# Performance work log

Hardware: AMD Instinct MI355X
Metric: run time of the kernel (lower is better)

Reference implementation:

```python
import jax, jax.numpy as jnp
import numpy as np

B, S, E, H = 64, 512, 768, 256


def setup_inputs() -> dict:
    key = jax.random.key(0)
    ks = jax.random.split(key, 9)
    sc = 0.02  # small init so relu-activated LSTM stays numerically sane
    x = jax.random.normal(ks[0], (B, S, E), dtype=jnp.float32)
    kernel_f = jax.random.normal(ks[1], (E, 4 * H), dtype=jnp.float32) * sc
    rec_f = jax.random.normal(ks[2], (H, 4 * H), dtype=jnp.float32) * sc
    bias_f = jnp.zeros((4 * H,), dtype=jnp.float32)
    kernel_b = jax.random.normal(ks[3], (E, 4 * H), dtype=jnp.float32) * sc
    rec_b = jax.random.normal(ks[4], (H, 4 * H), dtype=jnp.float32) * sc
    bias_b = jnp.zeros((4 * H,), dtype=jnp.float32)
    Wd = jax.random.normal(ks[5], (S * H, 2), dtype=jnp.float32) * sc
    bd = jnp.zeros((2,), dtype=jnp.float32)
    return {"x": x, "kernel_f": kernel_f, "rec_f": rec_f, "bias_f": bias_f,
            "kernel_b": kernel_b, "rec_b": rec_b, "bias_b": bias_b,
            "Wd": Wd, "bd": bd}


def _lstm_relu(x, kernel, rec, bias):
    # Keras LSTM with activation='relu', recurrent_activation='sigmoid'.
    # Gate order in keras kernel: [i, f, c, o].
    b, h = x.shape[0], rec.shape[0]
    xz = jnp.einsum('bse,eg->bsg', x, kernel) + bias  # [B,S,4H] precomputed input part

    def step(carry, zt):
        hp, cp = carry
        z = zt + hp @ rec  # [B,4H]
        zi, zf, zc, zo = jnp.split(z, 4, axis=-1)
        i = jax.nn.sigmoid(zi)
        f = jax.nn.sigmoid(zf)
        o = jax.nn.sigmoid(zo)
        c = f * cp + i * jax.nn.relu(zc)
        hn = o * jax.nn.relu(c)
        return (hn, c), hn

    init = (jnp.zeros((b, h), x.dtype), jnp.zeros((b, h), x.dtype))
    _, hs = jax.lax.scan(step, init, jnp.swapaxes(xz, 0, 1))  # [S,B,H]
    return jnp.swapaxes(hs, 0, 1)  # [B,S,H]


def reference(x, kernel_f, rec_f, bias_f, kernel_b, rec_b, bias_b, Wd, bd):
    h_fwd = _lstm_relu(x, kernel_f, rec_f, bias_f)
    # backward direction: process reversed sequence, reverse output back, then merge_mode='sum'
    h_bwd = _lstm_relu(x[:, ::-1], kernel_b, rec_b, bias_b)[:, ::-1]
    h = h_fwd + h_bwd  # [B,S,H]
    # dropout is identity at inference (training=None)
    flat = h.reshape(h.shape[0], -1)  # [B, S*H]
    logits = flat @ Wd + bd  # [B,2]
    return logits
```

## Files before the change

### kernel.cpp

```cpp
#include <hip/hip_runtime.h>
#include <hip/hip_bf16.h>
#include <hip/hip_fp16.h>

#define B_ 64
#define S_ 512
#define E_ 768
#define H_ 256
#define G_ 1024
#define MROWS 32768

typedef float f32x4 __attribute__((ext_vector_type(4)));
typedef float f32x16 __attribute__((ext_vector_type(16)));
typedef short short8 __attribute__((ext_vector_type(8)));
typedef _Float16 v2h __attribute__((ext_vector_type(2)));
typedef unsigned int u32x4 __attribute__((ext_vector_type(4)));


__global__ void cast_x_kernel(const float* __restrict__ x, __hip_bfloat16* __restrict__ xbf, int n) {
    int i = (blockIdx.x * 256 + threadIdx.x) * 4;
    if (i >= n) return;
    float4 v = *(const float4*)(x + i);
    xbf[i + 0] = __float2bfloat16(v.x);
    xbf[i + 1] = __float2bfloat16(v.y);
    xbf[i + 2] = __float2bfloat16(v.z);
    xbf[i + 3] = __float2bfloat16(v.w);
}

__global__ void prep_kT_kernel(const float* __restrict__ kf, const float* __restrict__ kb,
                               __hip_bfloat16* __restrict__ kT) {
    int idx = blockIdx.x * 256 + threadIdx.x;
    int dir = blockIdx.y;
    const float* src = dir ? kb : kf;
    int k = idx >> 10;
    int n = idx & 1023;
    float v = src[idx];
    kT[(size_t)dir * G_ * E_ + (size_t)n * E_ + k] = __float2bfloat16(v);
}

__global__ void prep_recQ_kernel(const float* __restrict__ rf, const float* __restrict__ rb,
                                 unsigned int* __restrict__ recQ) {
    int idx = blockIdx.x * 256 + threadIdx.x;
    int dir = blockIdx.y;
    const float* src = dir ? rb : rf;
    int g  = idx & 1023;
    int u  = (idx >> 10) & 3;
    int kk = idx >> 12;
    int k0 = 8 * kk + 2 * u;
    float a = src[(size_t)k0 * G_ + g];
    float b = src[(size_t)(k0 + 1) * G_ + g];
    v2h p;
    p[0] = (_Float16)a;
    p[1] = (_Float16)b;
    recQ[(size_t)dir * 131072 + (size_t)kk * 4096 + g * 4 + u] = __builtin_bit_cast(unsigned int, p);
}

#define TM 128
#define TN 128
#define BK 32
#define LDA 40

__global__ __launch_bounds__(256) void gemm_xz_kernel(
        const __hip_bfloat16* __restrict__ xbf,
        const __hip_bfloat16* __restrict__ kT,
        const float* __restrict__ bias_f, const float* __restrict__ bias_b,
        __hip_bfloat16* __restrict__ xz) {
    int dir  = blockIdx.z;
    int nblk = blockIdx.x;
    int mblk = blockIdx.y;
    int tid  = threadIdx.x;
    int wave = tid >> 6, lane = tid & 63;

    __shared__ __hip_bfloat16 shA[TM * LDA];
    __shared__ __hip_bfloat16 shB[TN * LDA];

    int m0 = mblk * TM;
    int n0 = nblk * TN;

    int rowl0 = tid >> 2;
    int rowl1 = rowl0 + 64;
    int k8    = (tid & 3) * 8;
    int ar0 = m0 + rowl0, ar1 = m0 + rowl1;
    int sa0 = (ar0 & ~511) | (dir ? (511 - (ar0 & 511)) : (ar0 & 511));
    int sa1 = (ar1 & ~511) | (dir ? (511 - (ar1 & 511)) : (ar1 & 511));
    const __hip_bfloat16* kbase = kT + (size_t)dir * G_ * E_;

    f32x16 acc[4] = {};

    int lm = lane & 31;
    int kq = (lane >> 5) * 8;

    for (int k0 = 0; k0 < E_; k0 += BK) {
        __syncthreads();
        *(short8*)&shA[rowl0 * LDA + k8] = *(const short8*)(xbf + (size_t)sa0 * E_ + k0 + k8);
        *(short8*)&shA[rowl1 * LDA + k8] = *(const short8*)(xbf + (size_t)sa1 * E_ + k0 + k8);
        *(short8*)&shB[rowl0 * LDA + k8] = *(const short8*)(kbase + (size_t)(n0 + rowl0) * E_ + k0 + k8);
        *(short8*)&shB[rowl1 * LDA + k8] = *(const short8*)(kbase + (size_t)(n0 + rowl1) * E_ + k0 + k8);
        __syncthreads();

#pragma unroll
        for (int kk = 0; kk < BK; kk += 16) {
            short8 afrag = *(const short8*)&shA[(wave * 32 + lm) * LDA + kk + kq];
#pragma unroll
            for (int j = 0; j < 4; ++j) {
                short8 bfrag = *(const short8*)&shB[(j * 32 + lm) * LDA + kk + kq];
                acc[j] = __builtin_amdgcn_mfma_f32_32x32x16_bf16(afrag, bfrag, acc[j], 0, 0, 0);
            }
        }
    }

    const float* bias = dir ? bias_b : bias_f;
#pragma unroll
    for (int j = 0; j < 4; ++j) {
        int col = n0 + j * 32 + lm;
        float bv = bias[col];
#pragma unroll
        for (int reg = 0; reg < 16; ++reg) {
            int row = m0 + wave * 32 + (reg & 3) + 8 * (reg >> 2) + 4 * (lane >> 5);
            xz[((size_t)dir * MROWS + row) * G_ + col] = __float2bfloat16(acc[j][reg] + bv);
        }
    }
}

__device__ inline float dot2f16(unsigned int rbits, unsigned int hbits, float acc) {
#if __has_builtin(__builtin_amdgcn_fdot2)
    return __builtin_amdgcn_fdot2(__builtin_bit_cast(v2h, rbits),
                                  __builtin_bit_cast(v2h, hbits), acc, false);
#else
    v2h r = __builtin_bit_cast(v2h, rbits);
    v2h h = __builtin_bit_cast(v2h, hbits);
    return acc + (float)r[0] * (float)h[0] + (float)r[1] * (float)h[1];
#endif
}

__device__ inline float sigmoidf(float x) { return 1.f / (1.f + __expf(-x)); }

#define KKREG 24
#define KKLDS 8
__global__ __launch_bounds__(512) void scan_kernel(
        const __hip_bfloat16* __restrict__ xz,
        const uint4* __restrict__ recQ,
        const float* __restrict__ Wd,
        const float* __restrict__ bd,
        float* __restrict__ out) {
    int b = blockIdx.x, dir = blockIdx.y, tid = threadIdx.x;
    __shared__ __align__(16) uint4 sh_rec[KKLDS * G_];
    __shared__ __align__(16) _Float16 sh_h[2][H_];
    __shared__ float sh_z[G_];
    __shared__ float rbuf[8];

    const uint4* rqbase = recQ + (size_t)dir * 32768;

    u32x4 rr0[KKREG], rr1[KKREG];
    {
        unsigned long long a0 = (unsigned long long)(const void*)(rqbase + tid);
        unsigned long long a1 = (unsigned long long)(const void*)(rqbase + tid + 512);
#pragma unroll
        for (int kk = 0; kk < KKREG; ++kk) {
            unsigned long long ka0 = a0 + (unsigned long long)kk * 16384ull;
            unsigned long long ka1 = a1 + (unsigned long long)kk * 16384ull;
            asm volatile("global_load_dwordx4 %0, %1, off" : "=v"(rr0[kk]) : "v"(ka0));
            asm volatile("global_load_dwordx4 %0, %1, off" : "=v"(rr1[kk]) : "v"(ka1));
        }
        asm volatile("s_waitcnt vmcnt(0)" ::: "memory");
    }

#pragma unroll
    for (int j = 0; j < KKLDS * 2; ++j)
        sh_rec[j * 512 + tid] = rqbase[KKREG * 1024 + j * 512 + tid];

    if (tid < H_) { sh_h[0][tid] = (_Float16)0.f; }
    float c = 0.f, pl0 = 0.f, pl1 = 0.f;
    const __hip_bfloat16* xzb = xz + ((size_t)dir * MROWS + (size_t)b * S_) * G_ + tid;
    __syncthreads();

    int p = 0;
    for (int s = 0; s < S_; ++s) {
        float xz0 = __bfloat162float(xzb[(size_t)s * G_]);
        float xz1 = __bfloat162float(xzb[(size_t)s * G_ + 512]);
        float2 wv = {0.f, 0.f};
        int t = dir ? (S_ - 1 - s) : s;
        if (tid < H_) wv = ((const float2*)Wd)[t * H_ + tid];

        const uint4* hp = (const uint4*)&sh_h[p][0];
        float z0a = 0.f, z0b = 0.f, z1a = 0.f, z1b = 0.f;

#pragma unroll
        for (int kk = 0; kk < KKREG; ++kk) {
            uint4 hv = hp[kk];
            u32x4 r0 = rr0[kk];
            u32x4 r1 = rr1[kk];
            z0a = dot2f16(r0.x, hv.x, z0a); z0b = dot2f16(r0.y, hv.y, z0b);
            z0a = dot2f16(r0.z, hv.z, z0a); z0b = dot2f16(r0.w, hv.w, z0b);
            z1a = dot2f16(r1.x, hv.x, z1a); z1b = dot2f16(r1.y, hv.y, z1b);
            z1a = dot2f16(r1.z, hv.z, z1a); z1b = dot2f16(r1.w, hv.w, z1b);
        }
#pragma unroll
        for (int j = 0; j < KKLDS; ++j) {
            uint4 hv = hp[KKREG + j];
            uint4 r0 = sh_rec[j * 1024 + tid];
            uint4 r1 = sh_rec[j * 1024 + tid + 512];
            z0a = dot2f16(r0.x, hv.x, z0a); z0b = dot2f16(r0.y, hv.y, z0b);
            z0a = dot2f16(r0.z, hv.z, z0a); z0b = dot2f16(r0.w, hv.w, z0b);
            z1a = dot2f16(r1.x, hv.x, z1a); z1b = dot2f16(r1.y, hv.y, z1b);
            z1a = dot2f16(r1.z, hv.z, z1a); z1b = dot2f16(r1.w, hv.w, z1b);
        }
        sh_z[tid]       = z0a + z0b + xz0;
        sh_z[tid + 512] = z1a + z1b + xz1;
        __syncthreads();

        if (tid < H_) {
            float zi = sh_z[tid];
            float zf = sh_z[H_ + tid];
            float zc = sh_z[2 * H_ + tid];
            float zo = sh_z[3 * H_ + tid];
            float ig = sigmoidf(zi);
            float fg = sigmoidf(zf);
            float og = sigmoidf(zo);
            float cc = fmaxf(zc, 0.f);
            c = fg * c + ig * cc;
            float h = og * fmaxf(c, 0.f);
            sh_h[p ^ 1][tid] = (_Float16)h;

            pl0 = fmaf(h, wv.x, pl0);
            pl1 = fmaf(h, wv.y, pl1);
        }
        __syncthreads();
        p ^= 1;
    }

    if (tid < H_) {
#pragma unroll
        for (int off = 32; off > 0; off >>= 1) {
            pl0 += __shfl_down(pl0, off);
            pl1 += __shfl_down(pl1, off);
        }
    }
    if (tid < H_ && (tid & 63) == 0) {
        int w = tid >> 6;
        rbuf[w] = pl0; rbuf[4 + w] = pl1;
    }
    __syncthreads();
    if (tid == 0) {
        float t0 = rbuf[0] + rbuf[1] + rbuf[2] + rbuf[3];
        float t1 = rbuf[4] + rbuf[5] + rbuf[6] + rbuf[7];
        atomicAdd(&out[b * 2 + 0], t0);
        atomicAdd(&out[b * 2 + 1], t1);
    }
    if (dir == 0 && tid < 2) atomicAdd(&out[b * 2 + tid], bd[tid]);
}

extern "C" void kernel_launch(void* const* d_in, const int* in_sizes, int n_in,
                              void* d_out, int out_size, void* d_ws, size_t ws_size,
                              hipStream_t stream) {
    const float* x        = (const float*)d_in[0];
    const float* kernel_f = (const float*)d_in[1];
    const float* rec_f    = (const float*)d_in[2];
    const float* bias_f   = (const float*)d_in[3];
    const float* kernel_b = (const float*)d_in[4];
    const float* rec_b    = (const float*)d_in[5];
    const float* bias_b   = (const float*)d_in[6];
    const float* Wd       = (const float*)d_in[7];
    const float* bd       = (const float*)d_in[8];
    float* out = (float*)d_out;

    char* w = (char*)d_ws;
    __hip_bfloat16* xz  = (__hip_bfloat16*)w;
    __hip_bfloat16* xbf = (__hip_bfloat16*)(w + 134217728);
    __hip_bfloat16* kT  = (__hip_bfloat16*)(w + 184549376);
    unsigned int*  recQ = (unsigned int*) (w + 187695104);

    int nx = B_ * S_ * E_;
    cast_x_kernel<<<nx / (256 * 4), 256, 0, stream>>>(x, xbf, nx);
    prep_kT_kernel<<<dim3((E_ * G_) / 256, 2), 256, 0, stream>>>(kernel_f, kernel_b, kT);
    prep_recQ_kernel<<<dim3(131072 / 256, 2), 256, 0, stream>>>(rec_f, rec_b, recQ);

    gemm_xz_kernel<<<dim3(G_ / TN, MROWS / TM, 2), 256, 0, stream>>>(xbf, kT, bias_f, bias_b, xz);

    hipMemsetAsync(d_out, 0, (size_t)out_size * sizeof(float), stream);
    scan_kernel<<<dim3(B_, 2), 512, 0, stream>>>(xz, (const uint4*)recQ, Wd, bd, out);
}
```

Measured before the change: 1.191 ms.

## Compute all four gates per thread in scan, pinning weights in AGPRs

The recurrent scan block shrinks from 512 to 256 threads, and each thread now computes all four gate pre-activations for one hidden unit. This removes the sh_z shared-memory exchange and one of the two barriers per timestep. To hold the larger per-thread weight slice, it is split across VGPRs (11 k-chunks), AGPRs accessed through inline accvgpr write/read (14 chunks), and LDS (7 chunks), which cuts LDS reads of weights. The cost is twice as many dot products per thread on half the threads, plus an extra accvgpr read before each AGPR-held weight is used.

```diff
diff --git a/kernel.cpp b/kernel.cpp
--- a/kernel.cpp
+++ b/kernel.cpp
@@ -134,108 +134,145 @@
 
 __device__ inline float sigmoidf(float x) { return 1.f / (1.f + __expf(-x)); }
 
-#define KKREG 24
-#define KKLDS 8
-__global__ __launch_bounds__(512) void scan_kernel(
+__device__ inline unsigned apin(unsigned v) {
+    unsigned a;
+    asm volatile("v_accvgpr_write_b32 %0, %1" : "=a"(a) : "v"(v));
+    return a;
+}
+__device__ inline unsigned aread(unsigned a) {
+    unsigned v;
+    asm volatile("v_accvgpr_read_b32 %0, %1" : "=v"(v) : "a"(a));
+    return v;
+}
+
+#define KKV 11
+#define KKA 14
+#define KKL 7
+__global__ __launch_bounds__(256) __attribute__((amdgpu_waves_per_eu(1)))
+void scan_kernel(
         const __hip_bfloat16* __restrict__ xz,
         const uint4* __restrict__ recQ,
         const float* __restrict__ Wd,
         const float* __restrict__ bd,
         float* __restrict__ out) {
     int b = blockIdx.x, dir = blockIdx.y, tid = threadIdx.x;
-    __shared__ __align__(16) uint4 sh_rec[KKLDS * G_];
+    __shared__ __align__(16) uint4 sh_rec[KKL * G_];
     __shared__ __align__(16) _Float16 sh_h[2][H_];
-    __shared__ float sh_z[G_];
     __shared__ float rbuf[8];
 
     const uint4* rqbase = recQ + (size_t)dir * 32768;
 
-    u32x4 rr0[KKREG], rr1[KKREG];
+    u32x4 vi[KKV], vf[KKV], vc[KKV], vo[KKV];
     {
-        unsigned long long a0 = (unsigned long long)(const void*)(rqbase + tid);
-        unsigned long long a1 = (unsigned long long)(const void*)(rqbase + tid + 512);
-#pragma unroll
-        for (int kk = 0; kk < KKREG; ++kk) {
-            unsigned long long ka0 = a0 + (unsigned long long)kk * 16384ull;
-            unsigned long long ka1 = a1 + (unsigned long long)kk * 16384ull;
-            asm volatile("global_load_dwordx4 %0, %1, off" : "=v"(rr0[kk]) : "v"(ka0));
-            asm volatile("global_load_dwordx4 %0, %1, off" : "=v"(rr1[kk]) : "v"(ka1));
+        unsigned long long ai = (unsigned long long)(const void*)(rqbase + tid);
+        unsigned long long af = (unsigned long long)(const void*)(rqbase + tid + 256);
+        unsigned long long ac = (unsigned long long)(const void*)(rqbase + tid + 512);
+        unsigned long long ao = (unsigned long long)(const void*)(rqbase + tid + 768);
+#pragma unroll
+        for (int kk = 0; kk < KKV; ++kk) {
+            unsigned long long o = (unsigned long long)kk * 16384ull;
+            asm volatile("global_load_dwordx4 %0, %1, off" : "=v"(vi[kk]) : "v"(ai + o));
+            asm volatile("global_load_dwordx4 %0, %1, off" : "=v"(vf[kk]) : "v"(af + o));
+            asm volatile("global_load_dwordx4 %0, %1, off" : "=v"(vc[kk]) : "v"(ac + o));
+            asm volatile("global_load_dwordx4 %0, %1, off" : "=v"(vo[kk]) : "v"(ao + o));
         }
         asm volatile("s_waitcnt vmcnt(0)" ::: "memory");
     }
 
-#pragma unroll
-    for (int j = 0; j < KKLDS * 2; ++j)
-        sh_rec[j * 512 + tid] = rqbase[KKREG * 1024 + j * 512 + tid];
-
-    if (tid < H_) { sh_h[0][tid] = (_Float16)0.f; }
+    unsigned agi[KKA][4], agf[KKA][4], agc[KKA][4], ago[KKA][4];
+#pragma unroll
+    for (int kk = 0; kk < KKA; ++kk) {
+        const uint4* g = rqbase + (KKV + kk) * 1024 + tid;
+        uint4 ti = g[0], tf = g[256], tc = g[512], to = g[768];
+        agi[kk][0] = apin(ti.x); agi[kk][1] = apin(ti.y); agi[kk][2] = apin(ti.z); agi[kk][3] = apin(ti.w);
+        agf[kk][0] = apin(tf.x); agf[kk][1] = apin(tf.y); agf[kk][2] = apin(tf.z); agf[kk][3] = apin(tf.w);
+        agc[kk][0] = apin(tc.x); agc[kk][1] = apin(tc.y); agc[kk][2] = apin(tc.z); agc[kk][3] = apin(tc.w);
+        ago[kk][0] = apin(to.x); ago[kk][1] = apin(to.y); ago[kk][2] = apin(to.z); ago[kk][3] = apin(to.w);
+    }
+
+#pragma unroll
+    for (int j = 0; j < KKL * 4; ++j)
+        sh_rec[j * 256 + tid] = rqbase[(KKV + KKA) * 1024 + j * 256 + tid];
+
+    sh_h[0][tid] = (_Float16)0.f;
     float c = 0.f, pl0 = 0.f, pl1 = 0.f;
     const __hip_bfloat16* xzb = xz + ((size_t)dir * MROWS + (size_t)b * S_) * G_ + tid;
     __syncthreads();
 
     int p = 0;
     for (int s = 0; s < S_; ++s) {
-        float xz0 = __bfloat162float(xzb[(size_t)s * G_]);
-        float xz1 = __bfloat162float(xzb[(size_t)s * G_ + 512]);
-        float2 wv = {0.f, 0.f};
+        float xzi = __bfloat162float(xzb[(size_t)s * G_]);
+        float xzf = __bfloat162float(xzb[(size_t)s * G_ + 256]);
+        float xzc = __bfloat162float(xzb[(size_t)s * G_ + 512]);
+        float xzo = __bfloat162float(xzb[(size_t)s * G_ + 768]);
         int t = dir ? (S_ - 1 - s) : s;
-        if (tid < H_) wv = ((const float2*)Wd)[t * H_ + tid];
+        float2 wv = ((const float2*)Wd)[t * H_ + tid];
 
         const uint4* hp = (const uint4*)&sh_h[p][0];
-        float z0a = 0.f, z0b = 0.f, z1a = 0.f, z1b = 0.f;
-
-#pragma unroll
-        for (int kk = 0; kk < KKREG; ++kk) {
+        float zia = 0.f, zib = 0.f, zfa = 0.f, zfb = 0.f;
+        float zca = 0.f, zcb = 0.f, zoa = 0.f, zob = 0.f;
+
+#pragma unroll
+        for (int kk = 0; kk < KKV; ++kk) {
             uint4 hv = hp[kk];
-            u32x4 r0 = rr0[kk];
-            u32x4 r1 = rr1[kk];
-            z0a = dot2f16(r0.x, hv.x, z0a); z0b = dot2f16(r0.y, hv.y, z0b);
-            z0a = dot2f16(r0.z, hv.z, z0a); z0b = dot2f16(r0.w, hv.w, z0b);
-            z1a = dot2f16(r1.x, hv.x, z1a); z1b = dot2f16(r1.y, hv.y, z1b);
-            z1a = dot2f16(r1.z, hv.z, z1a); z1b = dot2f16(r1.w, hv.w, z1b);
-        }
-#pragma unroll
-        for (int j = 0; j < KKLDS; ++j) {
-            uint4 hv = hp[KKREG + j];
-            uint4 r0 = sh_rec[j * 1024 + tid];
-            uint4 r1 = sh_rec[j * 1024 + tid + 512];
-            z0a = dot2f16(r0.x, hv.x, z0a); z0b = dot2f16(r0.y, hv.y, z0b);
-            z0a = dot2f16(r0.z, hv.z, z0a); z0b = dot2f16(r0.w, hv.w, z0b);
-            z1a = dot2f16(r1.x, hv.x, z1a); z1b = dot2f16(r1.y, hv.y, z1b);
-            z1a = dot2f16(r1.z, hv.z, z1a); z1b = dot2f16(r1.w, hv.w, z1b);
-        }
-        sh_z[tid]       = z0a + z0b + xz0;
-        sh_z[tid + 512] = z1a + z1b + xz1;
-        __syncthreads();
-
-        if (tid < H_) {
-            float zi = sh_z[tid];
-            float zf = sh_z[H_ + tid];
-            float zc = sh_z[2 * H_ + tid];
-            float zo = sh_z[3 * H_ + tid];
-            float ig = sigmoidf(zi);
-            float fg = sigmoidf(zf);
-            float og = sigmoidf(zo);
-            float cc = fmaxf(zc, 0.f);
-            c = fg * c + ig * cc;
-            float h = og * fmaxf(c, 0.f);
-            sh_h[p ^ 1][tid] = (_Float16)h;
-
-            pl0 = fmaf(h, wv.x, pl0);
-            pl1 = fmaf(h, wv.y, pl1);
-        }
+            u32x4 ri = vi[kk], rf = vf[kk], rc = vc[kk], ro = vo[kk];
+            zia = dot2f16(ri.x, hv.x, zia); zib = dot2f16(ri.y, hv.y, zib);
+            zia = dot2f16(ri.z, hv.z, zia); zib = dot2f16(ri.w, hv.w, zib);
+            zfa = dot2f16(rf.x, hv.x, zfa); zfb = dot2f16(rf.y, hv.y, zfb);
+            zfa = dot2f16(rf.z, hv.z, zfa); zfb = dot2f16(rf.w, hv.w, zfb);
+            zca = dot2f16(rc.x, hv.x, zca); zcb = dot2f16(rc.y, hv.y, zcb);
+            zca = dot2f16(rc.z, hv.z, zca); zcb = dot2f16(rc.w, hv.w, zcb);
+            zoa = dot2f16(ro.x, hv.x, zoa); zob = dot2f16(ro.y, hv.y, zob);
+            zoa = dot2f16(ro.z, hv.z, zoa); zob = dot2f16(ro.w, hv.w, zob);
+        }
+#pragma unroll
+        for (int kk = 0; kk < KKA; ++kk) {
+            uint4 hv = hp[KKV + kk];
+            zia = dot2f16(aread(agi[kk][0]), hv.x, zia); zib = dot2f16(aread(agi[kk][1]), hv.y, zib);
+            zia = dot2f16(aread(agi[kk][2]), hv.z, zia); zib = dot2f16(aread(agi[kk][3]), hv.w, zib);
+            zfa = dot2f16(aread(agf[kk][0]), hv.x, zfa); zfb = dot2f16(aread(agf[kk][1]), hv.y, zfb);
+            zfa = dot2f16(aread(agf[kk][2]), hv.z, zfa); zfb = dot2f16(aread(agf[kk][3]), hv.w, zfb);
+            zca = dot2f16(aread(agc[kk][0]), hv.x, zca); zcb = dot2f16(aread(agc[kk][1]), hv.y, zcb);
+            zca = dot2f16(aread(agc[kk][2]), hv.z, zca); zcb = dot2f16(aread(agc[kk][3]), hv.w, zcb);
+            zoa = dot2f16(aread(ago[kk][0]), hv.x, zoa); zob = dot2f16(aread(ago[kk][1]), hv.y, zob);
+            zoa = dot2f16(aread(ago[kk][2]), hv.z, zoa); zob = dot2f16(aread(ago[kk][3]), hv.w, zob);
+        }
+#pragma unroll
+        for (int j = 0; j < KKL; ++j) {
+            uint4 hv = hp[KKV + KKA + j];
+            uint4 ri = sh_rec[j * 1024 + tid];
+            uint4 rf = sh_rec[j * 1024 + tid + 256];
+            uint4 rc = sh_rec[j * 1024 + tid + 512];
+            uint4 ro = sh_rec[j * 1024 + tid + 768];
+            zia = dot2f16(ri.x, hv.x, zia); zib = dot2f16(ri.y, hv.y, zib);
+            zia = dot2f16(ri.z, hv.z, zia); zib = dot2f16(ri.w, hv.w, zib);
+            zfa = dot2f16(rf.x, hv.x, zfa); zfb = dot2f16(rf.y, hv.y, zfb);
+            zfa = dot2f16(rf.z, hv.z, zfa); zfb = dot2f16(rf.w, hv.w, zfb);
+            zca = dot2f16(rc.x, hv.x, zca); zcb = dot2f16(rc.y, hv.y, zcb);
+            zca = dot2f16(rc.z, hv.z, zca); zcb = dot2f16(rc.w, hv.w, zcb);
+            zoa = dot2f16(ro.x, hv.x, zoa); zob = dot2f16(ro.y, hv.y, zob);
+            zoa = dot2f16(ro.z, hv.z, zoa); zob = dot2f16(ro.w, hv.w, zob);
+        }
+
+        float ig = sigmoidf(zia + zib + xzi);
+        float fg = sigmoidf(zfa + zfb + xzf);
+        float cc = fmaxf(zca + zcb + xzc, 0.f);
+        float og = sigmoidf(zoa + zob + xzo);
+        c = fg * c + ig * cc;
+        float h = og * fmaxf(c, 0.f);
+        sh_h[p ^ 1][tid] = (_Float16)h;
+        pl0 = fmaf(h, wv.x, pl0);
+        pl1 = fmaf(h, wv.y, pl1);
         __syncthreads();
         p ^= 1;
     }
 
-    if (tid < H_) {
-#pragma unroll
-        for (int off = 32; off > 0; off >>= 1) {
-            pl0 += __shfl_down(pl0, off);
-            pl1 += __shfl_down(pl1, off);
-        }
-    }
-    if (tid < H_ && (tid & 63) == 0) {
+#pragma unroll
+    for (int off = 32; off > 0; off >>= 1) {
+        pl0 += __shfl_down(pl0, off);
+        pl1 += __shfl_down(pl1, off);
+    }
+    if ((tid & 63) == 0) {
         int w = tid >> 6;
         rbuf[w] = pl0; rbuf[4 + w] = pl1;
     }
@@ -277,5 +314,5 @@
     gemm_xz_kernel<<<dim3(G_ / TN, MROWS / TM, 2), 256, 0, stream>>>(xbf, kT, bias_f, bias_b, xz);
 
     hipMemsetAsync(d_out, 0, (size_t)out_size * sizeof(float), stream);
-    scan_kernel<<<dim3(B_, 2), 512, 0, stream>>>(xz, (const uint4*)recQ, Wd, bd, out);
-}
+    scan_kernel<<<dim3(B_, 2), 256, 0, stream>>>(xz, (const uint4*)recQ, Wd, bd, out);
+}
```

New measurement: 1.314 ms. 1.1x slower.
